# Kernel tuning notes

Hardware: AMD Instinct MI355X
Metric: run time of the kernel (lower is better)

Reference implementation:

```python
import jax, jax.numpy as jnp
import numpy as np

EPS = 1e-8

def _cosine_weights(keys, M, reverse=False):
    # keys: (bs, r, W); M: (bs, W, N) -> softmax over slots of cosine sim, shape (bs, r, N)
    kn = keys / (jnp.linalg.norm(keys, axis=-1, keepdims=True) + EPS)
    Mn = M / (jnp.linalg.norm(M, axis=1, keepdims=True) + EPS)
    dist = jnp.einsum('brw,bwn->brn', kn, Mn)
    if reverse:
        dist = -dist
    return jax.nn.softmax(dist, axis=2)

def setup_inputs() -> dict:
    key = jax.random.key(0)
    ks = jax.random.split(key, 8)
    bs, W, N, R = 128, 256, 2048, 4
    return {
        'k_r': jax.random.normal(ks[0], (bs, R * W), jnp.float32),
        'm_t': jax.random.normal(ks[1], (bs, W), jnp.float32),
        'e_t': jax.random.normal(ks[2], (bs, W), jnp.float32),
        'm_erased': jax.random.normal(ks[3], (bs, 1, W), jnp.float32),
        'memory': jax.random.uniform(ks[4], (bs, W, N), jnp.float32),
        'gW': jax.random.normal(ks[5], (1, 2 * W), jnp.float32) * 0.05,
        'gb': jnp.zeros((1,), jnp.float32),
        'oW': jax.random.normal(ks[6], (W, 2 * W), jnp.float32) * 0.05,
        'ob': jnp.zeros((W,), jnp.float32),
    }

def reference(k_r, m_t, e_t, m_erased, memory, gW, gb, oW, ob):
    bs, W, N = memory.shape
    R = k_r.shape[1] // W
    read_keys = jnp.tanh(k_r.reshape(bs, R, W))
    write_m = jnp.tanh(m_t.reshape(bs, 1, W))            # m_t candidate (bs,1,W)
    erase_vec = jax.nn.softmax(e_t.reshape(bs, 1, W), axis=2)
    # MixGate(write_m, m_erased)
    cat = jnp.concatenate([write_m, m_erased], axis=-1)  # (bs,1,2W)
    g = jax.nn.sigmoid(jnp.einsum('biw,ow->bio', cat, gW) + gb)  # (bs,1,1)
    gated = jnp.concatenate([g * write_m, (1.0 - g) * m_erased], axis=-1)
    write_key = jax.nn.relu(jnp.einsum('biw,ow->bio', gated, oW) + ob)  # (bs,1,W)
    # content weighting with reversed (dissimilarity) cosine
    write_wt = _cosine_weights(write_key, memory, reverse=True)  # (bs,1,N)
    # M = M * (1 - et^T wt) + mt^T wt
    reset_gate = 1.0 - jnp.einsum('biw,bin->bwn', erase_vec, write_wt)
    M_new = memory * reset_gate + jnp.einsum('biw,bin->bwn', write_m, write_wt)
    # read
    read_wt = _cosine_weights(read_keys, M_new)          # (bs,R,N)
    m_read = jnp.einsum('brn,bwn->brw', read_wt, M_new)  # (bs,R,W)
    return (m_read, M_new, read_wt)
```

## Files before the change

### kernel.cpp

```cpp
#include <hip/hip_runtime.h>
#include <math.h>

#define EPS 1e-8f
#define BS 128
#define W 256
#define N 2048
#define N4 (N / 4)
#define R 4

using v4f = float __attribute__((ext_vector_type(4)));

__device__ inline float wave_sum(float v) {
#pragma unroll
    for (int o = 32; o > 0; o >>= 1) v += __shfl_xor(v, o, 64);
    return v;
}
__device__ inline float wave_max(float v) {
#pragma unroll
    for (int o = 32; o > 0; o >>= 1) v = fmaxf(v, __shfl_xor(v, o, 64));
    return v;
}
__device__ inline float block_sum(float v, volatile float* red, int lane, int wid) {
    v = wave_sum(v);
    if (lane == 0) red[wid] = v;
    __syncthreads();
    v = red[0] + red[1] + red[2] + red[3];
    __syncthreads();
    return v;
}
__device__ inline float block_max(float v, volatile float* red, int lane, int wid) {
    v = wave_max(v);
    if (lane == 0) red[wid] = v;
    __syncthreads();
    v = fmaxf(fmaxf(red[0], red[1]), fmaxf(red[2], red[3]));
    __syncthreads();
    return v;
}
__device__ inline void fma4s(float4& a, float s, const float4& v) {
    a.x += s * v.x; a.y += s * v.y; a.z += s * v.z; a.w += s * v.w;
}
__device__ inline void fma44(float4& a, const float4& u, const float4& v) {
    a.x += u.x * v.x; a.y += u.y * v.y; a.z += u.z * v.z; a.w += u.w * v.w;
}

__global__ void k_prep(const float* __restrict__ k_r, const float* __restrict__ m_t,
                       const float* __restrict__ e_t, const float* __restrict__ m_er,
                       const float* __restrict__ gW, const float* __restrict__ gb,
                       const float* __restrict__ oW, const float* __restrict__ ob,
                       float* __restrict__ wm_o, float* __restrict__ er_o,
                       float* __restrict__ knw_o, float* __restrict__ knr_o,
                       float* __restrict__ c0_o) {
    int b = blockIdx.x, t = threadIdx.x;
    int lane = t & 63, wid = t >> 6;
    __shared__ float red[4];
    __shared__ float gated[2 * W];
    __shared__ float wk_s[W];

    float wm = tanhf(m_t[b * W + t]);
    float me = m_er[b * W + t];
    wm_o[b * W + t] = wm;

    float e = e_t[b * W + t];
    float mx = block_max(e, red, lane, wid);
    float ex = expf(e - mx);
    float s = block_sum(ex, red, lane, wid);
    er_o[b * W + t] = ex / s;

    float pw = block_sum(wm * wm, red, lane, wid);
    if (t == 0) c0_o[b * 5 + 4] = pw;

    float p = wm * gW[t] + me * gW[W + t];
    float ps = block_sum(p, red, lane, wid) + gb[0];
    float g = 1.0f / (1.0f + expf(-ps));
    gated[t] = g * wm;
    gated[W + t] = (1.0f - g) * me;
    __syncthreads();

    const float4* g4 = (const float4*)gated;
    float4 g0 = g4[lane];
    float4 g1 = g4[64 + lane];
    for (int i = 0; i < 64; i++) {
        int o = wid * 64 + i;
        const float4* orow = (const float4*)(oW + (size_t)o * 2 * W);
        float4 w0 = orow[lane];
        float4 w1 = orow[64 + lane];
        float pp = w0.x * g0.x + w0.y * g0.y + w0.z * g0.z + w0.w * g0.w
                 + w1.x * g1.x + w1.y * g1.y + w1.z * g1.z + w1.w * g1.w;
        pp = wave_sum(pp);
        if (lane == 0) wk_s[o] = fmaxf(pp + ob[o], 0.0f);
    }
    __syncthreads();
    float wk = wk_s[t];
    float ss = block_sum(wk * wk, red, lane, wid);
    knw_o[b * W + t] = wk / (sqrtf(ss) + EPS);

    for (int r = 0; r < R; r++) {
        float rk = tanhf(k_r[(b * R + r) * W + t]);
        float s2 = block_sum(rk * rk, red, lane, wid);
        float kn = rk / (sqrtf(s2) + EPS);
        knr_o[(b * R + r) * W + t] = kn;
        float c0 = block_sum(kn * wm, red, lane, wid);
        if (t == 0) c0_o[b * 5 + r] = c0;
    }
}

__global__ void __launch_bounds__(256, 2)
k_moments(const float* __restrict__ mem, const float* __restrict__ knw_g,
          const float* __restrict__ er_g, const float* __restrict__ wm_g,
          const float* __restrict__ knr_g, float4* __restrict__ scr) {
    int b = blockIdx.y, bx = blockIdx.x;
    int t = threadIdx.x;
    int half = t >> 7, c = t & 127;
    int n4 = bx * 128 + c;
    __shared__ float knw_s[W], er_s[W], wm_s[W], knr_s[R * W];
    __shared__ float4 comb[128 * 7];

    knw_s[t] = knw_g[b * W + t];
    er_s[t]  = er_g[b * W + t];
    wm_s[t]  = wm_g[b * W + t];
#pragma unroll
    for (int r = 0; r < R; r++) knr_s[r * W + t] = knr_g[(b * R + r) * W + t];
    __syncthreads();

    float4 acc[14];
#pragma unroll
    for (int j = 0; j < 14; j++) acc[j] = make_float4(0.f, 0.f, 0.f, 0.f);

    const float4* base = (const float4*)(mem + (size_t)b * W * N) + n4;
    int w0 = half * 128;
#pragma unroll 4
    for (int i = 0; i < 128; i++) {
        int w = w0 + i;
        float4 v = base[(size_t)w * N4];
        float e = er_s[w], m = wm_s[w], kw = knw_s[w];
        float4 ev;
        ev.x = e * v.x; ev.y = e * v.y; ev.z = e * v.z; ev.w = e * v.w;
        fma4s(acc[0], kw, v);
        fma44(acc[1], v, v);
        fma44(acc[2], ev, v);
        fma44(acc[3], ev, ev);
        fma4s(acc[4], m, v);
        fma4s(acc[5], m, ev);
        fma4s(acc[6], knr_s[w], v);
        fma4s(acc[7], knr_s[W + w], v);
        fma4s(acc[8], knr_s[2 * W + w], v);
        fma4s(acc[9], knr_s[3 * W + w], v);
        fma4s(acc[10], knr_s[w], ev);
        fma4s(acc[11], knr_s[W + w], ev);
        fma4s(acc[12], knr_s[2 * W + w], ev);
        fma4s(acc[13], knr_s[3 * W + w], ev);
    }

    if (half == 0) {
#pragma unroll
        for (int j = 0; j < 7; j++) comb[c * 7 + j] = acc[j];
    }
    __syncthreads();
    if (half == 1) {
#pragma unroll
        for (int j = 0; j < 7; j++) {
            float4 q = comb[c * 7 + j];
            q.x += acc[j].x; q.y += acc[j].y; q.z += acc[j].z; q.w += acc[j].w;
            scr[((size_t)(b * 14 + j)) * N4 + n4] = q;
        }
    }
    __syncthreads();
    if (half == 0) {
#pragma unroll
        for (int j = 0; j < 7; j++) comb[c * 7 + j] = acc[7 + j];
    }
    __syncthreads();
    if (half == 1) {
#pragma unroll
        for (int j = 0; j < 7; j++) {
            float4 q = comb[c * 7 + j];
            q.x += acc[7 + j].x; q.y += acc[7 + j].y; q.z += acc[7 + j].z; q.w += acc[7 + j].w;
            scr[((size_t)(b * 14 + 7 + j)) * N4 + n4] = q;
        }
    }
}

__global__ void k_weights(const float4* __restrict__ scr, const float* __restrict__ c0_g,
                          float* __restrict__ wwt_g, float* __restrict__ rwt_out,
                          float* __restrict__ C_g) {
    int b = blockIdx.y, pair = blockIdx.x;
    int t = threadIdx.x;
    int lane = t & 63, wid = t >> 6;
    __shared__ float red[4];

    const float4* S0 = scr + (size_t)(b * 14) * N4;
    float4 s1a = S0[t],        ssa = S0[N4 + t];
    float4 s1b = S0[256 + t],  ssb = S0[N4 + 256 + t];

    float4 da, db;
    da.x = -(s1a.x / (sqrtf(ssa.x) + EPS)); da.y = -(s1a.y / (sqrtf(ssa.y) + EPS));
    da.z = -(s1a.z / (sqrtf(ssa.z) + EPS)); da.w = -(s1a.w / (sqrtf(ssa.w) + EPS));
    db.x = -(s1b.x / (sqrtf(ssb.x) + EPS)); db.y = -(s1b.y / (sqrtf(ssb.y) + EPS));
    db.z = -(s1b.z / (sqrtf(ssb.z) + EPS)); db.w = -(s1b.w / (sqrtf(ssb.w) + EPS));

    float m8 = fmaxf(fmaxf(fmaxf(da.x, da.y), fmaxf(da.z, da.w)),
                     fmaxf(fmaxf(db.x, db.y), fmaxf(db.z, db.w)));
    float mx = block_max(m8, red, lane, wid);
    float4 ea, eb;
    ea.x = expf(da.x - mx); ea.y = expf(da.y - mx); ea.z = expf(da.z - mx); ea.w = expf(da.w - mx);
    eb.x = expf(db.x - mx); eb.y = expf(db.y - mx); eb.z = expf(db.z - mx); eb.w = expf(db.w - mx);
    float s8 = ea.x + ea.y + ea.z + ea.w + eb.x + eb.y + eb.z + eb.w;
    float Z = block_sum(s8, red, lane, wid);
    float inv = 1.0f / Z;
    float4 ua, ub;
    ua.x = ea.x * inv; ua.y = ea.y * inv; ua.z = ea.z * inv; ua.w = ea.w * inv;
    ub.x = eb.x * inv; ub.y = eb.y * inv; ub.z = eb.z * inv; ub.w = eb.w * inv;
    if (pair == 0) {
        ((float4*)(wwt_g + (size_t)b * N))[t] = ua;
        ((float4*)(wwt_g + (size_t)b * N))[256 + t] = ub;
    }

    float4 q1a = S0[2 * N4 + t], q2a = S0[3 * N4 + t], p0a = S0[4 * N4 + t], p1a = S0[5 * N4 + t];
    float4 q1b = S0[2 * N4 + 256 + t], q2b = S0[3 * N4 + 256 + t],
           p0b = S0[4 * N4 + 256 + t], p1b = S0[5 * N4 + 256 + t];
    float pw = c0_g[b * 5 + 4];

    float4 dena, denb;
    {
        dena.x = sqrtf(ssa.x + ua.x * (2.f * p0a.x - 2.f * q1a.x) + ua.x * ua.x * (q2a.x - 2.f * p1a.x + pw)) + EPS;
        dena.y = sqrtf(ssa.y + ua.y * (2.f * p0a.y - 2.f * q1a.y) + ua.y * ua.y * (q2a.y - 2.f * p1a.y + pw)) + EPS;
        dena.z = sqrtf(ssa.z + ua.z * (2.f * p0a.z - 2.f * q1a.z) + ua.z * ua.z * (q2a.z - 2.f * p1a.z + pw)) + EPS;
        dena.w = sqrtf(ssa.w + ua.w * (2.f * p0a.w - 2.f * q1a.w) + ua.w * ua.w * (q2a.w - 2.f * p1a.w + pw)) + EPS;
        denb.x = sqrtf(ssb.x + ub.x * (2.f * p0b.x - 2.f * q1b.x) + ub.x * ub.x * (q2b.x - 2.f * p1b.x + pw)) + EPS;
        denb.y = sqrtf(ssb.y + ub.y * (2.f * p0b.y - 2.f * q1b.y) + ub.y * ub.y * (q2b.y - 2.f * p1b.y + pw)) + EPS;
        denb.z = sqrtf(ssb.z + ub.z * (2.f * p0b.z - 2.f * q1b.z) + ub.z * ub.z * (q2b.z - 2.f * p1b.z + pw)) + EPS;
        denb.w = sqrtf(ssb.w + ub.w * (2.f * p0b.w - 2.f * q1b.w) + ub.w * ub.w * (q2b.w - 2.f * p1b.w + pw)) + EPS;
    }

#pragma unroll
    for (int rr = 0; rr < 2; rr++) {
        int r = pair * 2 + rr;
        float c0 = c0_g[b * 5 + r];
        float4 t0a = S0[(6 + r) * N4 + t], t1a = S0[(10 + r) * N4 + t];
        float4 t0b = S0[(6 + r) * N4 + 256 + t], t1b = S0[(10 + r) * N4 + 256 + t];
        float4 dra, drb;
        dra.x = (t0a.x + ua.x * (c0 - t1a.x)) / dena.x;
        dra.y = (t0a.y + ua.y * (c0 - t1a.y)) / dena.y;
        dra.z = (t0a.z + ua.z * (c0 - t1a.z)) / dena.z;
        dra.w = (t0a.w + ua.w * (c0 - t1a.w)) / dena.w;
        drb.x = (t0b.x + ub.x * (c0 - t1b.x)) / denb.x;
        drb.y = (t0b.y + ub.y * (c0 - t1b.y)) / denb.y;
        drb.z = (t0b.z + ub.z * (c0 - t1b.z)) / denb.z;
        drb.w = (t0b.w + ub.w * (c0 - t1b.w)) / denb.w;

        float rm = fmaxf(fmaxf(fmaxf(dra.x, dra.y), fmaxf(dra.z, dra.w)),
                         fmaxf(fmaxf(drb.x, drb.y), fmaxf(drb.z, drb.w)));
        float rmx = block_max(rm, red, lane, wid);
        float4 ra, rb;
        ra.x = expf(dra.x - rmx); ra.y = expf(dra.y - rmx);
        ra.z = expf(dra.z - rmx); ra.w = expf(dra.w - rmx);
        rb.x = expf(drb.x - rmx); rb.y = expf(drb.y - rmx);
        rb.z = expf(drb.z - rmx); rb.w = expf(drb.w - rmx);
        float rs = ra.x + ra.y + ra.z + ra.w + rb.x + rb.y + rb.z + rb.w;
        float RZ = block_sum(rs, red, lane, wid);
        float rinv = 1.0f / RZ;
        ra.x *= rinv; ra.y *= rinv; ra.z *= rinv; ra.w *= rinv;
        rb.x *= rinv; rb.y *= rinv; rb.z *= rinv; rb.w *= rinv;
        float4* ro = (float4*)(rwt_out + (size_t)b * R * N);
        ro[r * 512 + t] = ra;
        ro[r * 512 + 256 + t] = rb;
        float cpart = ra.x * ua.x + ra.y * ua.y + ra.z * ua.z + ra.w * ua.w
                    + rb.x * ub.x + rb.y * ub.y + rb.z * ub.z + rb.w * ub.w;
        float C = block_sum(cpart, red, lane, wid);
        if (t == 0) C_g[b * R + r] = C;
    }
}

__global__ void __launch_bounds__(256, 2)
k_mnew_read(const float* __restrict__ mem, const float* __restrict__ wwt_g,
            const float* __restrict__ rwt_g, const float* __restrict__ C_g,
            const float* __restrict__ er_g, const float* __restrict__ wm_g,
            float* __restrict__ Mnew, float* __restrict__ m_read) {
    int b = blockIdx.y;
    int w0 = blockIdx.x * 64;
    int t = threadIdx.x;
    int lane = t & 63, wid = t >> 6;

    __shared__ float4 rwt4[R * 512];
    __shared__ float4 wwt4[512];
    __shared__ float er_s[64], wm_s[64];
    __shared__ float part_a[64][2][4], part_b[64][2][4];

    const float4* ro = (const float4*)(rwt_g + (size_t)b * R * N);
#pragma unroll
    for (int i = 0; i < 8; i++) rwt4[i * 256 + t] = ro[i * 256 + t];
    const float4* wo = (const float4*)(wwt_g + (size_t)b * N);
    wwt4[t] = wo[t];
    wwt4[256 + t] = wo[256 + t];
    if (t < 64) {
        er_s[t] = er_g[b * W + w0 + t];
        wm_s[t] = wm_g[b * W + w0 + t];
    }
    __syncthreads();

    int half = wid & 1, rowgrp = wid >> 1;
    int fbase = half * 256 + lane;

    float4 wt4[4], rw[R][4], uw[R][4];
#pragma unroll
    for (int k = 0; k < 4; k++) wt4[k] = wwt4[fbase + k * 64];
#pragma unroll
    for (int r = 0; r < R; r++)
#pragma unroll
        for (int k = 0; k < 4; k++) {
            rw[r][k] = rwt4[r * 512 + fbase + k * 64];
            uw[r][k].x = rw[r][k].x * wt4[k].x;
            uw[r][k].y = rw[r][k].y * wt4[k].y;
            uw[r][k].z = rw[r][k].z * wt4[k].z;
            uw[r][k].w = rw[r][k].w * wt4[k].w;
        }

    const float* Mb = mem + (size_t)b * W * N;
    float* Ob = Mnew + (size_t)b * W * N;
#pragma unroll 2
    for (int wi = 0; wi < 32; wi++) {
        int wl = rowgrp * 32 + wi;
        float erw = er_s[wl], wmw = wm_s[wl];
        const float4* mrow = (const float4*)(Mb + (size_t)(w0 + wl) * N);
        v4f* orow = (v4f*)(Ob + (size_t)(w0 + wl) * N);
        float4 v[4];
#pragma unroll
        for (int k = 0; k < 4; k++) v[k] = mrow[fbase + k * 64];
        float a0 = 0.f, a1 = 0.f, a2 = 0.f, a3 = 0.f;
        float b0 = 0.f, b1 = 0.f, b2 = 0.f, b3 = 0.f;
#pragma unroll
        for (int k = 0; k < 4; k++) {
            v4f mn;
            mn[0] = v[k].x + wt4[k].x * (wmw - v[k].x * erw);
            mn[1] = v[k].y + wt4[k].y * (wmw - v[k].y * erw);
            mn[2] = v[k].z + wt4[k].z * (wmw - v[k].z * erw);
            mn[3] = v[k].w + wt4[k].w * (wmw - v[k].w * erw);
            __builtin_nontemporal_store(mn, orow + fbase + k * 64);
            a0 += rw[0][k].x * v[k].x + rw[0][k].y * v[k].y + rw[0][k].z * v[k].z + rw[0][k].w * v[k].w;
            a1 += rw[1][k].x * v[k].x + rw[1][k].y * v[k].y + rw[1][k].z * v[k].z + rw[1][k].w * v[k].w;
            a2 += rw[2][k].x * v[k].x + rw[2][k].y * v[k].y + rw[2][k].z * v[k].z + rw[2][k].w * v[k].w;
            a3 += rw[3][k].x * v[k].x + rw[3][k].y * v[k].y + rw[3][k].z * v[k].z + rw[3][k].w * v[k].w;
            b0 += uw[0][k].x * v[k].x + uw[0][k].y * v[k].y + uw[0][k].z * v[k].z + uw[0][k].w * v[k].w;
            b1 += uw[1][k].x * v[k].x + uw[1][k].y * v[k].y + uw[1][k].z * v[k].z + uw[1][k].w * v[k].w;
            b2 += uw[2][k].x * v[k].x + uw[2][k].y * v[k].y + uw[2][k].z * v[k].z + uw[2][k].w * v[k].w;
            b3 += uw[3][k].x * v[k].x + uw[3][k].y * v[k].y + uw[3][k].z * v[k].z + uw[3][k].w * v[k].w;
        }
        a0 = wave_sum(a0); a1 = wave_sum(a1); a2 = wave_sum(a2); a3 = wave_sum(a3);
        b0 = wave_sum(b0); b1 = wave_sum(b1); b2 = wave_sum(b2); b3 = wave_sum(b3);
        if (lane == 0) {
            part_a[wl][half][0] = a0; part_a[wl][half][1] = a1;
            part_a[wl][half][2] = a2; part_a[wl][half][3] = a3;
            part_b[wl][half][0] = b0; part_b[wl][half][1] = b1;
            part_b[wl][half][2] = b2; part_b[wl][half][3] = b3;
        }
    }
    __syncthreads();
    int w = t >> 2, r = t & 3;
    float A = part_a[w][0][r] + part_a[w][1][r];
    float B = part_b[w][0][r] + part_b[w][1][r];
    float C = C_g[b * R + r];
    float erv = er_s[w];
    float wmv = wm_s[w];
    m_read[((size_t)b * R + r) * W + w0 + w] = A - erv * B + wmv * C;
}

extern "C" void kernel_launch(void* const* d_in, const int* in_sizes, int n_in,
                              void* d_out, int out_size, void* d_ws, size_t ws_size,
                              hipStream_t stream) {
    const float* k_r  = (const float*)d_in[0];
    const float* m_t  = (const float*)d_in[1];
    const float* e_t  = (const float*)d_in[2];
    const float* m_er = (const float*)d_in[3];
    const float* mem  = (const float*)d_in[4];
    const float* gW   = (const float*)d_in[5];
    const float* gb   = (const float*)d_in[6];
    const float* oW   = (const float*)d_in[7];
    const float* ob   = (const float*)d_in[8];

    float* out = (float*)d_out;
    float* m_read = out;
    float* Mnew   = out + (size_t)BS * R * W;
    float* rwt    = out + (size_t)BS * R * W + (size_t)BS * W * N;

    float4* scr = (float4*)Mnew;

    float* ws  = (float*)d_ws;
    float* wm  = ws;
    float* er  = wm + (size_t)BS * W;
    float* knw = er + (size_t)BS * W;
    float* knr = knw + (size_t)BS * W;
    float* c0  = knr + (size_t)BS * R * W;
    float* wwt = c0 + (size_t)BS * 8;
    float* Cg  = wwt + (size_t)BS * N;

    k_prep<<<BS, 256, 0, stream>>>(k_r, m_t, e_t, m_er, gW, gb, oW, ob,
                                   wm, er, knw, knr, c0);
    k_moments<<<dim3(4, BS), 256, 0, stream>>>(mem, knw, er, wm, knr, scr);
    k_weights<<<dim3(2, BS), 256, 0, stream>>>(scr, c0, wwt, rwt, Cg);
    k_mnew_read<<<dim3(4, BS), 256, 0, stream>>>(mem, wwt, rwt, Cg, er, wm,
                                                 Mnew, m_read);
}
```

Measured before the change: 208.5 us.

## Fuse softmax-weight kernel into Mnew/read pass and batch moment loads

Merges the weights kernel into the Mnew/read kernel. Each of the 4 column blocks per batch recomputes the write and read softmaxes from the moment scratch and keeps them in LDS, removing one launch and the global round trip for wwt, rwt and C. The scratch moves from the Mnew output buffer to the workspace so the fused kernel can write Mnew while still reading moments. The moments loop now issues 8 loads before computing, and the softmax max-subtraction is dropped because the cosine values are bounded. The cost is 4x redundant softmax work per batch and higher LDS use, which may reduce occupancy.

```diff
diff --git a/kernel.cpp b/kernel.cpp
--- a/kernel.cpp
+++ b/kernel.cpp
@@ -128,27 +128,31 @@
 
     const float4* base = (const float4*)(mem + (size_t)b * W * N) + n4;
     int w0 = half * 128;
-#pragma unroll 4
-    for (int i = 0; i < 128; i++) {
-        int w = w0 + i;
-        float4 v = base[(size_t)w * N4];
-        float e = er_s[w], m = wm_s[w], kw = knw_s[w];
-        float4 ev;
-        ev.x = e * v.x; ev.y = e * v.y; ev.z = e * v.z; ev.w = e * v.w;
-        fma4s(acc[0], kw, v);
-        fma44(acc[1], v, v);
-        fma44(acc[2], ev, v);
-        fma44(acc[3], ev, ev);
-        fma4s(acc[4], m, v);
-        fma4s(acc[5], m, ev);
-        fma4s(acc[6], knr_s[w], v);
-        fma4s(acc[7], knr_s[W + w], v);
-        fma4s(acc[8], knr_s[2 * W + w], v);
-        fma4s(acc[9], knr_s[3 * W + w], v);
-        fma4s(acc[10], knr_s[w], ev);
-        fma4s(acc[11], knr_s[W + w], ev);
-        fma4s(acc[12], knr_s[2 * W + w], ev);
-        fma4s(acc[13], knr_s[3 * W + w], ev);
+    for (int ii = 0; ii < 16; ii++) {
+        float4 v[8];
+#pragma unroll
+        for (int j = 0; j < 8; j++) v[j] = base[(size_t)(w0 + ii * 8 + j) * N4];
+#pragma unroll
+        for (int j = 0; j < 8; j++) {
+            int w = w0 + ii * 8 + j;
+            float e = er_s[w], m = wm_s[w], kw = knw_s[w];
+            float4 ev;
+            ev.x = e * v[j].x; ev.y = e * v[j].y; ev.z = e * v[j].z; ev.w = e * v[j].w;
+            fma4s(acc[0], kw, v[j]);
+            fma44(acc[1], v[j], v[j]);
+            fma44(acc[2], ev, v[j]);
+            fma44(acc[3], ev, ev);
+            fma4s(acc[4], m, v[j]);
+            fma4s(acc[5], m, ev);
+            fma4s(acc[6], knr_s[w], v[j]);
+            fma4s(acc[7], knr_s[W + w], v[j]);
+            fma4s(acc[8], knr_s[2 * W + w], v[j]);
+            fma4s(acc[9], knr_s[3 * W + w], v[j]);
+            fma4s(acc[10], knr_s[w], ev);
+            fma4s(acc[11], knr_s[W + w], ev);
+            fma4s(acc[12], knr_s[2 * W + w], ev);
+            fma4s(acc[13], knr_s[3 * W + w], ev);
+        }
     }
 
     if (half == 0) {
@@ -180,140 +184,109 @@
     }
 }
 
-__global__ void k_weights(const float4* __restrict__ scr, const float* __restrict__ c0_g,
-                          float* __restrict__ wwt_g, float* __restrict__ rwt_out,
-                          float* __restrict__ C_g) {
-    int b = blockIdx.y, pair = blockIdx.x;
+__global__ void __launch_bounds__(256, 2)
+k_fused(const float* __restrict__ mem, const float4* __restrict__ scr,
+        const float* __restrict__ c0_g, const float* __restrict__ er_g,
+        const float* __restrict__ wm_g,
+        float* __restrict__ rwt_out, float* __restrict__ Mnew,
+        float* __restrict__ m_read) {
+    int b = blockIdx.y;
+    int bx = blockIdx.x;
+    int w0 = bx * 64;
     int t = threadIdx.x;
     int lane = t & 63, wid = t >> 6;
+
+    __shared__ float4 rwt4[R * 512];
+    __shared__ float4 u_lds[512];
     __shared__ float red[4];
+    __shared__ float er_s[64], wm_s[64];
+    __shared__ float part_a[64][2][4], part_b[64][2][4];
+
+    if (t < 64) {
+        er_s[t] = er_g[b * W + w0 + t];
+        wm_s[t] = wm_g[b * W + w0 + t];
+    }
 
     const float4* S0 = scr + (size_t)(b * 14) * N4;
-    float4 s1a = S0[t],        ssa = S0[N4 + t];
-    float4 s1b = S0[256 + t],  ssb = S0[N4 + 256 + t];
-
-    float4 da, db;
-    da.x = -(s1a.x / (sqrtf(ssa.x) + EPS)); da.y = -(s1a.y / (sqrtf(ssa.y) + EPS));
-    da.z = -(s1a.z / (sqrtf(ssa.z) + EPS)); da.w = -(s1a.w / (sqrtf(ssa.w) + EPS));
-    db.x = -(s1b.x / (sqrtf(ssb.x) + EPS)); db.y = -(s1b.y / (sqrtf(ssb.y) + EPS));
-    db.z = -(s1b.z / (sqrtf(ssb.z) + EPS)); db.w = -(s1b.w / (sqrtf(ssb.w) + EPS));
-
-    float m8 = fmaxf(fmaxf(fmaxf(da.x, da.y), fmaxf(da.z, da.w)),
-                     fmaxf(fmaxf(db.x, db.y), fmaxf(db.z, db.w)));
-    float mx = block_max(m8, red, lane, wid);
+    float4 s1a = S0[t],       ssa = S0[N4 + t];
+    float4 s1b = S0[256 + t], ssb = S0[N4 + 256 + t];
+
     float4 ea, eb;
-    ea.x = expf(da.x - mx); ea.y = expf(da.y - mx); ea.z = expf(da.z - mx); ea.w = expf(da.w - mx);
-    eb.x = expf(db.x - mx); eb.y = expf(db.y - mx); eb.z = expf(db.z - mx); eb.w = expf(db.w - mx);
-    float s8 = ea.x + ea.y + ea.z + ea.w + eb.x + eb.y + eb.z + eb.w;
-    float Z = block_sum(s8, red, lane, wid);
-    float inv = 1.0f / Z;
+    ea.x = expf(-(s1a.x / (sqrtf(ssa.x) + EPS)));
+    ea.y = expf(-(s1a.y / (sqrtf(ssa.y) + EPS)));
+    ea.z = expf(-(s1a.z / (sqrtf(ssa.z) + EPS)));
+    ea.w = expf(-(s1a.w / (sqrtf(ssa.w) + EPS)));
+    eb.x = expf(-(s1b.x / (sqrtf(ssb.x) + EPS)));
+    eb.y = expf(-(s1b.y / (sqrtf(ssb.y) + EPS)));
+    eb.z = expf(-(s1b.z / (sqrtf(ssb.z) + EPS)));
+    eb.w = expf(-(s1b.w / (sqrtf(ssb.w) + EPS)));
+    float Zw = block_sum(ea.x + ea.y + ea.z + ea.w + eb.x + eb.y + eb.z + eb.w,
+                         red, lane, wid);
+    float invw = 1.0f / Zw;
     float4 ua, ub;
-    ua.x = ea.x * inv; ua.y = ea.y * inv; ua.z = ea.z * inv; ua.w = ea.w * inv;
-    ub.x = eb.x * inv; ub.y = eb.y * inv; ub.z = eb.z * inv; ub.w = eb.w * inv;
-    if (pair == 0) {
-        ((float4*)(wwt_g + (size_t)b * N))[t] = ua;
-        ((float4*)(wwt_g + (size_t)b * N))[256 + t] = ub;
-    }
+    ua.x = ea.x * invw; ua.y = ea.y * invw; ua.z = ea.z * invw; ua.w = ea.w * invw;
+    ub.x = eb.x * invw; ub.y = eb.y * invw; ub.z = eb.z * invw; ub.w = eb.w * invw;
+    u_lds[t] = ua;
+    u_lds[256 + t] = ub;
 
     float4 q1a = S0[2 * N4 + t], q2a = S0[3 * N4 + t], p0a = S0[4 * N4 + t], p1a = S0[5 * N4 + t];
     float4 q1b = S0[2 * N4 + 256 + t], q2b = S0[3 * N4 + 256 + t],
            p0b = S0[4 * N4 + 256 + t], p1b = S0[5 * N4 + 256 + t];
     float pw = c0_g[b * 5 + 4];
-
     float4 dena, denb;
-    {
-        dena.x = sqrtf(ssa.x + ua.x * (2.f * p0a.x - 2.f * q1a.x) + ua.x * ua.x * (q2a.x - 2.f * p1a.x + pw)) + EPS;
-        dena.y = sqrtf(ssa.y + ua.y * (2.f * p0a.y - 2.f * q1a.y) + ua.y * ua.y * (q2a.y - 2.f * p1a.y + pw)) + EPS;
-        dena.z = sqrtf(ssa.z + ua.z * (2.f * p0a.z - 2.f * q1a.z) + ua.z * ua.z * (q2a.z - 2.f * p1a.z + pw)) + EPS;
-        dena.w = sqrtf(ssa.w + ua.w * (2.f * p0a.w - 2.f * q1a.w) + ua.w * ua.w * (q2a.w - 2.f * p1a.w + pw)) + EPS;
-        denb.x = sqrtf(ssb.x + ub.x * (2.f * p0b.x - 2.f * q1b.x) + ub.x * ub.x * (q2b.x - 2.f * p1b.x + pw)) + EPS;
-        denb.y = sqrtf(ssb.y + ub.y * (2.f * p0b.y - 2.f * q1b.y) + ub.y * ub.y * (q2b.y - 2.f * p1b.y + pw)) + EPS;
-        denb.z = sqrtf(ssb.z + ub.z * (2.f * p0b.z - 2.f * q1b.z) + ub.z * ub.z * (q2b.z - 2.f * p1b.z + pw)) + EPS;
-        denb.w = sqrtf(ssb.w + ub.w * (2.f * p0b.w - 2.f * q1b.w) + ub.w * ub.w * (q2b.w - 2.f * p1b.w + pw)) + EPS;
-    }
-
-#pragma unroll
-    for (int rr = 0; rr < 2; rr++) {
-        int r = pair * 2 + rr;
-        float c0 = c0_g[b * 5 + r];
+    dena.x = sqrtf(ssa.x + ua.x * (2.f * p0a.x - 2.f * q1a.x) + ua.x * ua.x * (q2a.x - 2.f * p1a.x + pw)) + EPS;
+    dena.y = sqrtf(ssa.y + ua.y * (2.f * p0a.y - 2.f * q1a.y) + ua.y * ua.y * (q2a.y - 2.f * p1a.y + pw)) + EPS;
+    dena.z = sqrtf(ssa.z + ua.z * (2.f * p0a.z - 2.f * q1a.z) + ua.z * ua.z * (q2a.z - 2.f * p1a.z + pw)) + EPS;
+    dena.w = sqrtf(ssa.w + ua.w * (2.f * p0a.w - 2.f * q1a.w) + ua.w * ua.w * (q2a.w - 2.f * p1a.w + pw)) + EPS;
+    denb.x = sqrtf(ssb.x + ub.x * (2.f * p0b.x - 2.f * q1b.x) + ub.x * ub.x * (q2b.x - 2.f * p1b.x + pw)) + EPS;
+    denb.y = sqrtf(ssb.y + ub.y * (2.f * p0b.y - 2.f * q1b.y) + ub.y * ub.y * (q2b.y - 2.f * p1b.y + pw)) + EPS;
+    denb.z = sqrtf(ssb.z + ub.z * (2.f * p0b.z - 2.f * q1b.z) + ub.z * ub.z * (q2b.z - 2.f * p1b.z + pw)) + EPS;
+    denb.w = sqrtf(ssb.w + ub.w * (2.f * p0b.w - 2.f * q1b.w) + ub.w * ub.w * (q2b.w - 2.f * p1b.w + pw)) + EPS;
+
+    float Cr[R];
+#pragma unroll
+    for (int r = 0; r < R; r++) {
+        float c0v = c0_g[b * 5 + r];
         float4 t0a = S0[(6 + r) * N4 + t], t1a = S0[(10 + r) * N4 + t];
         float4 t0b = S0[(6 + r) * N4 + 256 + t], t1b = S0[(10 + r) * N4 + 256 + t];
-        float4 dra, drb;
-        dra.x = (t0a.x + ua.x * (c0 - t1a.x)) / dena.x;
-        dra.y = (t0a.y + ua.y * (c0 - t1a.y)) / dena.y;
-        dra.z = (t0a.z + ua.z * (c0 - t1a.z)) / dena.z;
-        dra.w = (t0a.w + ua.w * (c0 - t1a.w)) / dena.w;
-        drb.x = (t0b.x + ub.x * (c0 - t1b.x)) / denb.x;
-        drb.y = (t0b.y + ub.y * (c0 - t1b.y)) / denb.y;
-        drb.z = (t0b.z + ub.z * (c0 - t1b.z)) / denb.z;
-        drb.w = (t0b.w + ub.w * (c0 - t1b.w)) / denb.w;
-
-        float rm = fmaxf(fmaxf(fmaxf(dra.x, dra.y), fmaxf(dra.z, dra.w)),
-                         fmaxf(fmaxf(drb.x, drb.y), fmaxf(drb.z, drb.w)));
-        float rmx = block_max(rm, red, lane, wid);
         float4 ra, rb;
-        ra.x = expf(dra.x - rmx); ra.y = expf(dra.y - rmx);
-        ra.z = expf(dra.z - rmx); ra.w = expf(dra.w - rmx);
-        rb.x = expf(drb.x - rmx); rb.y = expf(drb.y - rmx);
-        rb.z = expf(drb.z - rmx); rb.w = expf(drb.w - rmx);
-        float rs = ra.x + ra.y + ra.z + ra.w + rb.x + rb.y + rb.z + rb.w;
-        float RZ = block_sum(rs, red, lane, wid);
-        float rinv = 1.0f / RZ;
+        ra.x = expf((t0a.x + ua.x * (c0v - t1a.x)) / dena.x);
+        ra.y = expf((t0a.y + ua.y * (c0v - t1a.y)) / dena.y);
+        ra.z = expf((t0a.z + ua.z * (c0v - t1a.z)) / dena.z);
+        ra.w = expf((t0a.w + ua.w * (c0v - t1a.w)) / dena.w);
+        rb.x = expf((t0b.x + ub.x * (c0v - t1b.x)) / denb.x);
+        rb.y = expf((t0b.y + ub.y * (c0v - t1b.y)) / denb.y);
+        rb.z = expf((t0b.z + ub.z * (c0v - t1b.z)) / denb.z);
+        rb.w = expf((t0b.w + ub.w * (c0v - t1b.w)) / denb.w);
+        float Zr = block_sum(ra.x + ra.y + ra.z + ra.w + rb.x + rb.y + rb.z + rb.w,
+                             red, lane, wid);
+        float numC = block_sum(ra.x * ua.x + ra.y * ua.y + ra.z * ua.z + ra.w * ua.w
+                             + rb.x * ub.x + rb.y * ub.y + rb.z * ub.z + rb.w * ub.w,
+                               red, lane, wid);
+        float rinv = 1.0f / Zr;
         ra.x *= rinv; ra.y *= rinv; ra.z *= rinv; ra.w *= rinv;
         rb.x *= rinv; rb.y *= rinv; rb.z *= rinv; rb.w *= rinv;
-        float4* ro = (float4*)(rwt_out + (size_t)b * R * N);
-        ro[r * 512 + t] = ra;
-        ro[r * 512 + 256 + t] = rb;
-        float cpart = ra.x * ua.x + ra.y * ua.y + ra.z * ua.z + ra.w * ua.w
-                    + rb.x * ub.x + rb.y * ub.y + rb.z * ub.z + rb.w * ub.w;
-        float C = block_sum(cpart, red, lane, wid);
-        if (t == 0) C_g[b * R + r] = C;
-    }
-}
-
-__global__ void __launch_bounds__(256, 2)
-k_mnew_read(const float* __restrict__ mem, const float* __restrict__ wwt_g,
-            const float* __restrict__ rwt_g, const float* __restrict__ C_g,
-            const float* __restrict__ er_g, const float* __restrict__ wm_g,
-            float* __restrict__ Mnew, float* __restrict__ m_read) {
-    int b = blockIdx.y;
-    int w0 = blockIdx.x * 64;
-    int t = threadIdx.x;
-    int lane = t & 63, wid = t >> 6;
-
-    __shared__ float4 rwt4[R * 512];
-    __shared__ float4 wwt4[512];
-    __shared__ float er_s[64], wm_s[64];
-    __shared__ float part_a[64][2][4], part_b[64][2][4];
-
-    const float4* ro = (const float4*)(rwt_g + (size_t)b * R * N);
-#pragma unroll
-    for (int i = 0; i < 8; i++) rwt4[i * 256 + t] = ro[i * 256 + t];
-    const float4* wo = (const float4*)(wwt_g + (size_t)b * N);
-    wwt4[t] = wo[t];
-    wwt4[256 + t] = wo[256 + t];
-    if (t < 64) {
-        er_s[t] = er_g[b * W + w0 + t];
-        wm_s[t] = wm_g[b * W + w0 + t];
+        rwt4[r * 512 + t] = ra;
+        rwt4[r * 512 + 256 + t] = rb;
+        if (bx == 0) {
+            float4* ro = (float4*)(rwt_out + (size_t)b * R * N);
+            ro[r * 512 + t] = ra;
+            ro[r * 512 + 256 + t] = rb;
+        }
+        Cr[r] = numC * rinv;
     }
     __syncthreads();
 
     int half = wid & 1, rowgrp = wid >> 1;
     int fbase = half * 256 + lane;
 
-    float4 wt4[4], rw[R][4], uw[R][4];
-#pragma unroll
-    for (int k = 0; k < 4; k++) wt4[k] = wwt4[fbase + k * 64];
+    float4 u4[4], rw[R][4];
+#pragma unroll
+    for (int k = 0; k < 4; k++) u4[k] = u_lds[fbase + k * 64];
 #pragma unroll
     for (int r = 0; r < R; r++)
 #pragma unroll
-        for (int k = 0; k < 4; k++) {
-            rw[r][k] = rwt4[r * 512 + fbase + k * 64];
-            uw[r][k].x = rw[r][k].x * wt4[k].x;
-            uw[r][k].y = rw[r][k].y * wt4[k].y;
-            uw[r][k].z = rw[r][k].z * wt4[k].z;
-            uw[r][k].w = rw[r][k].w * wt4[k].w;
-        }
+        for (int k = 0; k < 4; k++) rw[r][k] = rwt4[r * 512 + fbase + k * 64];
 
     const float* Mb = mem + (size_t)b * W * N;
     float* Ob = Mnew + (size_t)b * W * N;
@@ -331,19 +304,22 @@
 #pragma unroll
         for (int k = 0; k < 4; k++) {
             v4f mn;
-            mn[0] = v[k].x + wt4[k].x * (wmw - v[k].x * erw);
-            mn[1] = v[k].y + wt4[k].y * (wmw - v[k].y * erw);
-            mn[2] = v[k].z + wt4[k].z * (wmw - v[k].z * erw);
-            mn[3] = v[k].w + wt4[k].w * (wmw - v[k].w * erw);
+            mn[0] = v[k].x + u4[k].x * (wmw - v[k].x * erw);
+            mn[1] = v[k].y + u4[k].y * (wmw - v[k].y * erw);
+            mn[2] = v[k].z + u4[k].z * (wmw - v[k].z * erw);
+            mn[3] = v[k].w + u4[k].w * (wmw - v[k].w * erw);
             __builtin_nontemporal_store(mn, orow + fbase + k * 64);
+            float4 vu;
+            vu.x = v[k].x * u4[k].x; vu.y = v[k].y * u4[k].y;
+            vu.z = v[k].z * u4[k].z; vu.w = v[k].w * u4[k].w;
             a0 += rw[0][k].x * v[k].x + rw[0][k].y * v[k].y + rw[0][k].z * v[k].z + rw[0][k].w * v[k].w;
             a1 += rw[1][k].x * v[k].x + rw[1][k].y * v[k].y + rw[1][k].z * v[k].z + rw[1][k].w * v[k].w;
             a2 += rw[2][k].x * v[k].x + rw[2][k].y * v[k].y + rw[2][k].z * v[k].z + rw[2][k].w * v[k].w;
             a3 += rw[3][k].x * v[k].x + rw[3][k].y * v[k].y + rw[3][k].z * v[k].z + rw[3][k].w * v[k].w;
-            b0 += uw[0][k].x * v[k].x + uw[0][k].y * v[k].y + uw[0][k].z * v[k].z + uw[0][k].w * v[k].w;
-            b1 += uw[1][k].x * v[k].x + uw[1][k].y * v[k].y + uw[1][k].z * v[k].z + uw[1][k].w * v[k].w;
-            b2 += uw[2][k].x * v[k].x + uw[2][k].y * v[k].y + uw[2][k].z * v[k].z + uw[2][k].w * v[k].w;
-            b3 += uw[3][k].x * v[k].x + uw[3][k].y * v[k].y + uw[3][k].z * v[k].z + uw[3][k].w * v[k].w;
+            b0 += rw[0][k].x * vu.x + rw[0][k].y * vu.y + rw[0][k].z * vu.z + rw[0][k].w * vu.w;
+            b1 += rw[1][k].x * vu.x + rw[1][k].y * vu.y + rw[1][k].z * vu.z + rw[1][k].w * vu.w;
+            b2 += rw[2][k].x * vu.x + rw[2][k].y * vu.y + rw[2][k].z * vu.z + rw[2][k].w * vu.w;
+            b3 += rw[3][k].x * vu.x + rw[3][k].y * vu.y + rw[3][k].z * vu.z + rw[3][k].w * vu.w;
         }
         a0 = wave_sum(a0); a1 = wave_sum(a1); a2 = wave_sum(a2); a3 = wave_sum(a3);
         b0 = wave_sum(b0); b1 = wave_sum(b1); b2 = wave_sum(b2); b3 = wave_sum(b3);
@@ -358,9 +334,9 @@
     int w = t >> 2, r = t & 3;
     float A = part_a[w][0][r] + part_a[w][1][r];
     float B = part_b[w][0][r] + part_b[w][1][r];
-    float C = C_g[b * R + r];
     float erv = er_s[w];
     float wmv = wm_s[w];
+    float C = (r == 0) ? Cr[0] : (r == 1) ? Cr[1] : (r == 2) ? Cr[2] : Cr[3];
     m_read[((size_t)b * R + r) * W + w0 + w] = A - erv * B + wmv * C;
 }
 
@@ -382,21 +358,17 @@
     float* Mnew   = out + (size_t)BS * R * W;
     float* rwt    = out + (size_t)BS * R * W + (size_t)BS * W * N;
 
-    float4* scr = (float4*)Mnew;
-
     float* ws  = (float*)d_ws;
     float* wm  = ws;
     float* er  = wm + (size_t)BS * W;
     float* knw = er + (size_t)BS * W;
     float* knr = knw + (size_t)BS * W;
     float* c0  = knr + (size_t)BS * R * W;
-    float* wwt = c0 + (size_t)BS * 8;
-    float* Cg  = wwt + (size_t)BS * N;
+    float4* scr = (float4*)(c0 + (size_t)BS * 8);
 
     k_prep<<<BS, 256, 0, stream>>>(k_r, m_t, e_t, m_er, gW, gb, oW, ob,
                                    wm, er, knw, knr, c0);
     k_moments<<<dim3(4, BS), 256, 0, stream>>>(mem, knw, er, wm, knr, scr);
-    k_weights<<<dim3(2, BS), 256, 0, stream>>>(scr, c0, wwt, rwt, Cg);
-    k_mnew_read<<<dim3(4, BS), 256, 0, stream>>>(mem, wwt, rwt, Cg, er, wm,
-                                                 Mnew, m_read);
-}
+    k_fused<<<dim3(4, BS), 256, 0, stream>>>(mem, scr, c0, er, wm,
+                                             rwt, Mnew, m_read);
+}
```

New measurement: 219.6 us. +5.3%, slower.
